# Kernel tuning notes

Measured on AMD Instinct MI355X. Metric: run time of the kernel, lower is better.

## Reference

```python
import jax, jax.numpy as jnp
import numpy as np


def setup_inputs() -> dict:
    key = jax.random.key(0)
    k1, k2, k3, k4 = jax.random.split(key, 4)
    B, Cin, H, W = 16, 64, 96, 96
    D, O, KH, KW, S = 100, 256, 3, 3, 3
    x = jax.random.normal(k1, (B, Cin, H, W), dtype=jnp.float32)
    dictionary = jax.random.normal(k2, (D, Cin, KH, KW), dtype=jnp.float32) * 0.05
    lookup_coefficients = jax.random.normal(k3, (O, KH, KW, S), dtype=jnp.float32) * 0.1
    lookup_indices = jax.random.randint(k4, (O, KH, KW, S), 0, D, dtype=jnp.int64)
    return {
        "x": x,
        "dictionary": dictionary,
        "lookup_coefficients": lookup_coefficients,
        "lookup_indices": lookup_indices,
    }


def reference(x, dictionary, lookup_coefficients, lookup_indices):
    # Dense conv with the small dictionary: [B, Cin, H, W] x [D, Cin, kh, kw] -> [B, D, Oh, Ow]
    conv_out = jax.lax.conv_general_dilated(
        x, dictionary,
        window_strides=(1, 1),
        padding=((1, 1), (1, 1)),
        dimension_numbers=("NCHW", "OIHW", "NCHW"),
    )
    O = lookup_coefficients.shape[0]
    D = dictionary.shape[0]
    # Flatten kernel-position and sparsity axes: each (position, slot) contributes
    # coeff * conv_out[:, idx] to output channel o; COO duplicates sum.
    idx = lookup_indices.reshape(O, -1)      # [O, P*S]
    coeff = lookup_coefficients.reshape(O, -1)  # [O, P*S]
    # Scatter-add into a per-output-channel weight over dictionary entries: W[o, d]
    Wmat = jnp.zeros((O, D), dtype=conv_out.dtype).at[jnp.arange(O)[:, None], idx].add(coeff)
    # Gather-weighted-sum == sparse (O x D) matmul against conv_out channels
    out = jnp.einsum("od,bdhw->bohw", Wmat, conv_out)
    return out
```

## Files before the change

kernel.cpp:

```cpp
#include <hip/hip_runtime.h>

#define NB   16
#define CIN  64
#define HH   96
#define WW   96
#define DD   100
#define OO   256
#define NWG  (NB * HH)
#define NCV  1536
#define WPAD 50

typedef __attribute__((ext_vector_type(8))) short  bf16x8;
typedef __attribute__((ext_vector_type(4))) float  f32x4;

#define FSWZ(wp) ((((wp) ^ ((wp) >> 3)) & 7) << 4)

static __device__ __forceinline__ unsigned short f32_to_bf16(float f) {
    unsigned int u = __float_as_uint(f);
    u += 0x7FFFu + ((u >> 16) & 1u);
    return (unsigned short)(u >> 16);
}

__global__ __launch_bounds__(256) void prep_kernel(
    const float* __restrict__ x, const float* __restrict__ dict,
    const float* __restrict__ coeff, const int* __restrict__ idx,
    unsigned short* __restrict__ x2, unsigned short* __restrict__ weff2,
    unsigned short* __restrict__ zbuf)
{
    __shared__ unsigned short lds[CIN * 100];
    __shared__ float wrow[DD];
    const int blk = blockIdx.x, tid = threadIdx.x;

    if (blk < NWG) {
        const int b = blk / HH, h = blk % HH;
        for (int it = 0; it < 6; ++it) {
            int i = tid + it * 256;
            int c = i / 24, w4 = i % 24;
            float4 v = *reinterpret_cast<const float4*>(
                x + (((size_t)(b * CIN + c) * HH + h) * WW + w4 * 4));
            ushort4 u;
            u.x = f32_to_bf16(v.x); u.y = f32_to_bf16(v.y);
            u.z = f32_to_bf16(v.z); u.w = f32_to_bf16(v.w);
            *reinterpret_cast<ushort4*>(&lds[c * 100 + w4 * 4]) = u;
        }
        __syncthreads();
        for (int it = 0; it < 6; ++it) {
            int i = tid + it * 256;
            int w = i / 16, c = (i % 16) * 4;
            ushort4 u;
            u.x = lds[(c + 0) * 100 + w];
            u.y = lds[(c + 1) * 100 + w];
            u.z = lds[(c + 2) * 100 + w];
            u.w = lds[(c + 3) * 100 + w];
            *reinterpret_cast<ushort4*>(x2 + (((size_t)(b * HH + h) * WW + w) * CIN + c)) = u;
        }
    } else {
        const int o = blk - NWG;
        if (o == 0 && tid < 8) zbuf[tid] = 0;
        if (tid < DD) wrow[tid] = 0.f;
        __syncthreads();
        if (tid == 0) {
            for (int s = 0; s < 27; ++s) wrow[idx[o * 27 + s]] += coeff[o * 27 + s];
        }
        __syncthreads();
        for (int j = tid; j < 576; j += 256) {
            int kpos = j >> 6, c = j & 63;
            float s = 0.f;
            for (int d = 0; d < DD; ++d)
                s += wrow[d] * dict[d * 576 + c * 9 + kpos];
            int otile = o >> 4, ks = c >> 5;
            int lane8 = (o & 15) | (((c >> 3) & 3) << 4);
            weff2[((size_t)(kpos * 32 + otile * 2 + ks)) * 512 + lane8 * 8 + (c & 7)]
                = f32_to_bf16(s);
        }
    }
}

__global__ __launch_bounds__(256, 2) void conv_kernel(
    const unsigned short* __restrict__ x2,
    const unsigned short* __restrict__ weff2,
    const unsigned short* __restrict__ zbuf,
    float* __restrict__ out)
{
    __shared__ unsigned short xs[4 * WPAD * 64];

    const int wg  = blockIdx.x;
    const int swz = (wg & 7) * (NCV / 8) + (wg >> 3);
    const int b = swz / 96, rem = swz % 96;
    const int hp = rem >> 1, wh = rem & 1;
    const int h0 = hp * 2, ws = wh * 48;
    const int tid = threadIdx.x;
    const int lane = tid & 63, wn = tid >> 6;
    const int l15 = lane & 15;

    char* xsb = reinterpret_cast<char*>(xs);
    const char* x2b = reinterpret_cast<const char*>(x2) + (size_t)b * HH * WW * 128;
    const char* zbp = reinterpret_cast<const char*>(zbuf);

    const unsigned short* wbase = weff2 + (size_t)(wn * 8) * 512 + lane * 8;
    bf16x8 bfr[3][4];
#pragma unroll
    for (int s = 0; s < 3; ++s) {
        const int off = (s >> 1) * 32 + (s & 1);
#pragma unroll
        for (int n = 0; n < 4; ++n)
            bfr[s][n] = *reinterpret_cast<const bf16x8*>(wbase + (off + n * 2) * 512);
    }

#pragma unroll
    for (int it = 0; it < 7; ++it) {
        int chunk = tid + it * 256;
        if (chunk < 1600) {
            int r = chunk / 400, rem2 = chunk % 400;
            int wp = rem2 >> 3, gb = (rem2 & 7) << 4;
            int hx = h0 - 1 + r, w = ws - 1 + wp;
            const char* src = (w >= 0 && w < WW && hx >= 0 && hx < HH)
                ? x2b + ((size_t)(hx * WW + w) * 128 + (gb ^ FSWZ(wp)))
                : zbp;
            __builtin_amdgcn_global_load_lds(
                (const __attribute__((address_space(1))) void*)src,
                (__attribute__((address_space(3))) void*)(xsb + chunk * 16),
                16, 0, 0);
        }
    }

    f32x4 acc[2][3][4];
#pragma unroll
    for (int q = 0; q < 2; ++q)
#pragma unroll
        for (int m = 0; m < 3; ++m)
#pragma unroll
            for (int n = 0; n < 4; ++n)
                acc[q][m][n] = (f32x4){0.f, 0.f, 0.f, 0.f};

    __syncthreads();

    bf16x8 ax[3][2][3];
#pragma unroll
    for (int p = 0; p < 2; ++p) {
        const int cbp = ((p & 1) * 32 + (lane >> 4) * 8) * 2;
#pragma unroll
        for (int q = 0; q < 2; ++q)
#pragma unroll
            for (int m = 0; m < 3; ++m) {
                int wpos = m * 16 + l15;
                ax[p][q][m] = *reinterpret_cast<const bf16x8*>(
                    xsb + q * 6400 + wpos * 128 + (cbp ^ FSWZ(wpos)));
            }
    }

#pragma unroll
    for (int s = 0; s < 18; ++s) {
        if (s < 16) {
            const int s2 = s + 2;
            const int kpos2 = s2 >> 1, ks2 = s2 & 1;
            const int kh2 = kpos2 / 3, dw2 = kpos2 % 3;
            const int cb2 = (ks2 * 32 + (lane >> 4) * 8) * 2;
#pragma unroll
            for (int q = 0; q < 2; ++q)
#pragma unroll
                for (int m = 0; m < 3; ++m) {
                    int wpos = m * 16 + l15 + dw2;
                    ax[s2 % 3][q][m] = *reinterpret_cast<const bf16x8*>(
                        xsb + (kh2 + q) * 6400 + wpos * 128 + (cb2 ^ FSWZ(wpos)));
                }
        }
        __builtin_amdgcn_s_setprio(1);
#pragma unroll
        for (int q = 0; q < 2; ++q)
#pragma unroll
            for (int m = 0; m < 3; ++m)
#pragma unroll
                for (int n = 0; n < 4; ++n)
                    acc[q][m][n] = __builtin_amdgcn_mfma_f32_16x16x32_bf16(
                        ax[s % 3][q][m], bfr[s % 3][n], acc[q][m][n], 0, 0, 0);
        __builtin_amdgcn_s_setprio(0);
        if (s < 15) {
            const int s3 = s + 3;
            const int off = (s3 >> 1) * 32 + (s3 & 1);
#pragma unroll
            for (int n = 0; n < 4; ++n)
                bfr[s % 3][n] = *reinterpret_cast<const bf16x8*>(
                    wbase + (off + n * 2) * 512);
        }
    }

#pragma unroll
    for (int q = 0; q < 2; ++q)
#pragma unroll
        for (int m = 0; m < 3; ++m)
#pragma unroll
            for (int n = 0; n < 4; ++n) {
                int o = wn * 64 + n * 16 + l15;
                int w = ws + m * 16 + (lane >> 4) * 4;
                *reinterpret_cast<f32x4*>(
                    out + (((size_t)(b * OO + o) * HH + h0 + q) * WW + w))
                    = acc[q][m][n];
            }
}

extern "C" void kernel_launch(void* const* d_in, const int* in_sizes, int n_in,
                              void* d_out, int out_size, void* d_ws, size_t ws_size,
                              hipStream_t stream) {
    const float* x     = (const float*)d_in[0];
    const float* dict  = (const float*)d_in[1];
    const float* coeff = (const float*)d_in[2];
    const int*   idx   = (const int*)d_in[3];
    float* out = (float*)d_out;

    char* ws = (char*)d_ws;
    unsigned short* weff2 = (unsigned short*)ws;
    unsigned short* zbuf  = (unsigned short*)(ws + 294912);
    unsigned short* x2    = (unsigned short*)(ws + 1048576);

    prep_kernel<<<NWG + OO, 256, 0, stream>>>(x, dict, coeff, idx, x2, weff2, zbuf);
    conv_kernel<<<NCV, 256, 0, stream>>>(x2, weff2, zbuf, out);
}
```

Before: 69.81 us.

## Cut register pressure in conv kernel for three workgroups per CU

New measurement: 226.4 us. 224% more time.

```diff
diff --git a/kernel.cpp b/kernel.cpp
--- a/kernel.cpp
+++ b/kernel.cpp
@@ -13,7 +13,7 @@
 typedef __attribute__((ext_vector_type(8))) short  bf16x8;
 typedef __attribute__((ext_vector_type(4))) float  f32x4;
 
-#define FSWZ(wp) ((((wp) ^ ((wp) >> 3)) & 7) << 4)
+#define FSWZ(wp) (((wp) & 7) << 4)
 
 static __device__ __forceinline__ unsigned short f32_to_bf16(float f) {
     unsigned int u = __float_as_uint(f);
@@ -76,7 +76,7 @@
     }
 }
 
-__global__ __launch_bounds__(256, 2) void conv_kernel(
+__global__ __launch_bounds__(256, 3) void conv_kernel(
     const unsigned short* __restrict__ x2,
     const unsigned short* __restrict__ weff2,
     const unsigned short* __restrict__ zbuf,
@@ -98,14 +98,13 @@
     const char* zbp = reinterpret_cast<const char*>(zbuf);
 
     const unsigned short* wbase = weff2 + (size_t)(wn * 8) * 512 + lane * 8;
-    bf16x8 bfr[3][4];
-#pragma unroll
-    for (int s = 0; s < 3; ++s) {
-        const int off = (s >> 1) * 32 + (s & 1);
-#pragma unroll
-        for (int n = 0; n < 4; ++n)
-            bfr[s][n] = *reinterpret_cast<const bf16x8*>(wbase + (off + n * 2) * 512);
-    }
+    bf16x8 bA[4], bB[4];
+#pragma unroll
+    for (int n = 0; n < 4; ++n)
+        bA[n] = *reinterpret_cast<const bf16x8*>(wbase + (n * 2 + 0) * 512);
+#pragma unroll
+    for (int n = 0; n < 4; ++n)
+        bB[n] = *reinterpret_cast<const bf16x8*>(wbase + (n * 2 + 1) * 512);
 
 #pragma unroll
     for (int it = 0; it < 7; ++it) {
@@ -135,53 +134,39 @@
 
     __syncthreads();
 
-    bf16x8 ax[3][2][3];
-#pragma unroll
-    for (int p = 0; p < 2; ++p) {
-        const int cbp = ((p & 1) * 32 + (lane >> 4) * 8) * 2;
+#pragma unroll
+    for (int s = 0; s < 18; ++s) {
+        const int kpos = s >> 1, ks = s & 1;
+        const int kh = kpos / 3, dw = kpos % 3;
+        const int cb = (ks * 32 + (lane >> 4) * 8) * 2;
+        bf16x8 a[2][3];
+#pragma unroll
+        for (int m = 0; m < 3; ++m) {
+            int wpos = m * 16 + l15 + dw;
+            int rowoff = wpos * 128 + (cb ^ FSWZ(wpos));
+#pragma unroll
+            for (int q = 0; q < 2; ++q)
+                a[q][m] = *reinterpret_cast<const bf16x8*>(
+                    xsb + (kh + q) * 6400 + rowoff);
+        }
+        __builtin_amdgcn_s_setprio(1);
 #pragma unroll
         for (int q = 0; q < 2; ++q)
 #pragma unroll
-            for (int m = 0; m < 3; ++m) {
-                int wpos = m * 16 + l15;
-                ax[p][q][m] = *reinterpret_cast<const bf16x8*>(
-                    xsb + q * 6400 + wpos * 128 + (cbp ^ FSWZ(wpos)));
-            }
-    }
-
-#pragma unroll
-    for (int s = 0; s < 18; ++s) {
+            for (int m = 0; m < 3; ++m)
+#pragma unroll
+                for (int n = 0; n < 4; ++n)
+                    acc[q][m][n] = __builtin_amdgcn_mfma_f32_16x16x32_bf16(
+                        a[q][m], (s & 1) ? bB[n] : bA[n], acc[q][m][n], 0, 0, 0);
+        __builtin_amdgcn_s_setprio(0);
         if (s < 16) {
             const int s2 = s + 2;
-            const int kpos2 = s2 >> 1, ks2 = s2 & 1;
-            const int kh2 = kpos2 / 3, dw2 = kpos2 % 3;
-            const int cb2 = (ks2 * 32 + (lane >> 4) * 8) * 2;
-#pragma unroll
-            for (int q = 0; q < 2; ++q)
-#pragma unroll
-                for (int m = 0; m < 3; ++m) {
-                    int wpos = m * 16 + l15 + dw2;
-                    ax[s2 % 3][q][m] = *reinterpret_cast<const bf16x8*>(
-                        xsb + (kh2 + q) * 6400 + wpos * 128 + (cb2 ^ FSWZ(wpos)));
-                }
-        }
-        __builtin_amdgcn_s_setprio(1);
-#pragma unroll
-        for (int q = 0; q < 2; ++q)
-#pragma unroll
-            for (int m = 0; m < 3; ++m)
-#pragma unroll
-                for (int n = 0; n < 4; ++n)
-                    acc[q][m][n] = __builtin_amdgcn_mfma_f32_16x16x32_bf16(
-                        ax[s % 3][q][m], bfr[s % 3][n], acc[q][m][n], 0, 0, 0);
-        __builtin_amdgcn_s_setprio(0);
-        if (s < 15) {
-            const int s3 = s + 3;
-            const int off = (s3 >> 1) * 32 + (s3 & 1);
-#pragma unroll
-            for (int n = 0; n < 4; ++n)
-                bfr[s % 3][n] = *reinterpret_cast<const bf16x8*>(
-                    wbase + (off + n * 2) * 512);
+            const int off = (s2 >> 1) * 32 + (s2 & 1);
+#pragma unroll
+            for (int n = 0; n < 4; ++n) {
+                bf16x8 v = *reinterpret_cast<const bf16x8*>(wbase + (off + n * 2) * 512);
+                if ((s & 1) == 0) bA[n] = v; else bB[n] = v;
+            }
         }
     }
 
```
